# Kernel optimization log

Hardware: AMD Instinct MI355X
Metric: run time of the kernel (lower is better)

## Reference

```python
import jax, jax.numpy as jnp
import numpy as np

HIGHEST = jax.lax.Precision.HIGHEST
KEY_CHUNK_SIZE = 4096 * 4  # hard-coded in the module's __call__
HEADS = 8
DIM_HEAD = 64


def _query_chunk_size(num_q: int) -> int:
    # replicates the module's static chunk-size selection
    if num_q % 64 == 0:
        return num_q // 64
    if num_q % 16 == 0:
        return num_q // 16
    if num_q % 4 == 0:
        return num_q // 4
    return num_q


def _me_attention(q, k, v, q_chunk: int, k_chunk: int):
    # q, k, v: (S, H, D) where H here is the flattened batch*heads axis
    S, H, D = q.shape
    num_kv = k.shape[0]
    k_chunk = min(k_chunk, num_kv)
    q = q / jnp.sqrt(jnp.asarray(D, q.dtype))
    kc = k.reshape(-1, k_chunk, H, D)          # (nk, kc, H, D)
    vc = v.reshape(-1, k_chunk, H, v.shape[-1])

    def per_qchunk(qch):  # qch: (qc, H, D)
        def summarize(args):
            kch, vch = args
            s = jnp.einsum('qhd,khd->qhk', qch, kch, precision=HIGHEST)
            m = jax.lax.stop_gradient(jnp.max(s, axis=-1, keepdims=True))
            e = jnp.exp(s - m)
            ev = jnp.einsum('khf,qhk->qhf', vch, e, precision=HIGHEST)
            return ev, e.sum(axis=-1), m[..., 0]
        evs, ews, ms = jax.lax.map(summarize, (kc, vc))  # stacked over key chunks
        gm = jnp.max(ms, axis=0)                # (qc, H) global running max
        sc = jnp.exp(ms - gm)                   # (nk, qc, H) rescale factors
        num = (evs * sc[..., None]).sum(axis=0)
        den = (ews * sc).sum(axis=0)
        return num / den[..., None]

    qs = q.reshape(-1, q_chunk, H, D)
    out = jax.lax.map(per_qchunk, qs)           # (nq, qc, H, F)
    return out.reshape(S, H, -1)


def _forward(hidden_states, w_q, w_k, w_v, w_out, b_out):
    B, S, Dm = hidden_states.shape
    H, dh = HEADS, DIM_HEAD
    q = hidden_states @ w_q
    k = hidden_states @ w_k
    v = hidden_states @ w_v

    def to_heads(t):  # (B,S,H*dh) -> (B*H, S, dh)
        return t.reshape(B, S, H, dh).transpose(0, 2, 1, 3).reshape(B * H, S, dh)

    qs, ks, vs = to_heads(q), to_heads(k), to_heads(v)
    # module transposes to (S, B*H, dh) before memory-efficient attention
    qcs = _query_chunk_size(S)
    attn = _me_attention(qs.transpose(1, 0, 2), ks.transpose(1, 0, 2),
                         vs.transpose(1, 0, 2), qcs, KEY_CHUNK_SIZE)
    attn = attn.transpose(1, 0, 2)  # (B*H, S, dh)
    attn = attn.reshape(B, H, S, dh).transpose(0, 2, 1, 3).reshape(B, S, H * dh)
    return attn @ w_out + b_out


def setup_inputs() -> dict:
    key = jax.random.key(0)
    ks = jax.random.split(key, 6)
    B, S, Dm = 2, 8192, 512
    inner = HEADS * DIM_HEAD  # 512
    return {
        'hidden_states': jax.random.normal(ks[0], (B, S, Dm), dtype=jnp.float32),
        'w_q': jax.random.normal(ks[1], (Dm, inner), dtype=jnp.float32) * 0.02,
        'w_k': jax.random.normal(ks[2], (Dm, inner), dtype=jnp.float32) * 0.02,
        'w_v': jax.random.normal(ks[3], (Dm, inner), dtype=jnp.float32) * 0.02,
        'w_out': jax.random.normal(ks[4], (inner, Dm), dtype=jnp.float32) * 0.02,
        'b_out': jnp.zeros((Dm,), dtype=jnp.float32),
    }


def reference(hidden_states, w_q, w_k, w_v, w_out, b_out):
    return _forward(hidden_states, w_q, w_k, w_v, w_out, b_out)
```

## Files before the change

kernel.cpp:

```cpp
#include <hip/hip_runtime.h>
#include <stdint.h>

typedef unsigned short u16;
typedef __attribute__((ext_vector_type(8))) short short8;
typedef __attribute__((ext_vector_type(4))) short short4v;
typedef __attribute__((ext_vector_type(4))) float f32x4;

#define MFMA16(a, b, c) __builtin_amdgcn_mfma_f32_16x16x16bf16_1k(a, b, c, 0, 0, 0)
#define MFMA32(a, b, c) __builtin_amdgcn_mfma_f32_16x16x32_bf16(a, b, c, 0, 0, 0)

#if __has_builtin(__builtin_amdgcn_exp2f)
#define EXP2F(x) __builtin_amdgcn_exp2f(x)
#else
#define EXP2F(x) exp2f(x)
#endif

#define ASYNC16(G, L)                                                            \
    __builtin_amdgcn_global_load_lds((const __attribute__((address_space(1))) void*)(const void*)(G), \
                                     (__attribute__((address_space(3))) void*)(void*)(L), 16, 0, 0)

__device__ __forceinline__ u16 f2bf(float f) {
    union { float f; uint32_t u; } c; c.f = f;
    uint32_t r = (c.u + 0x7fffu + ((c.u >> 16) & 1u)) >> 16;
    return (u16)r;
}

__global__ __launch_bounds__(256) void k_convert_x(const float* __restrict__ X, u16* __restrict__ Xb) {
    int idx = blockIdx.x * 256 + threadIdx.x;
    float4 v = ((const float4*)X)[idx];
    union { u16 s[4]; uint2 v; } u;
    u.s[0] = f2bf(v.x); u.s[1] = f2bf(v.y); u.s[2] = f2bf(v.z); u.s[3] = f2bf(v.w);
    ((uint2*)Xb)[idx] = u.v;
}

__global__ __launch_bounds__(256) void k_convert_w(const float* __restrict__ W0, const float* __restrict__ W1,
                                                   const float* __restrict__ W2, const float* __restrict__ W3,
                                                   u16* __restrict__ Wt) {
    __shared__ u16 T[64][72];
    const float* W = (blockIdx.z == 0) ? W0 : (blockIdx.z == 1) ? W1 : (blockIdx.z == 2) ? W2 : W3;
    int k0 = blockIdx.x * 64, n0 = blockIdx.y * 64;
    int t = threadIdx.x;
    for (int i = 0; i < 4; i++) {
        int id = t + i * 256;
        int row = id >> 4, c4 = (id & 15) * 4;
        float4 v = *(const float4*)(W + (size_t)(k0 + row) * 512 + n0 + c4);
        union { u16 s[4]; uint2 v; } u;
        u.s[0] = f2bf(v.x); u.s[1] = f2bf(v.y); u.s[2] = f2bf(v.z); u.s[3] = f2bf(v.w);
        *(uint2*)&T[row][c4] = u.v;
    }
    __syncthreads();
    u16* O = Wt + (size_t)blockIdx.z * 512 * 512;
    for (int i = 0; i < 2; i++) {
        int id = t + i * 256;
        int row = id >> 3, c8 = (id & 7) * 8;
        union { u16 s[8]; uint4 v; } tmp;
        for (int j = 0; j < 8; j++) tmp.s[j] = T[c8 + j][row];
        *(uint4*)(O + (size_t)(n0 + row) * 512 + k0 + c8) = tmp.v;
    }
}

__global__ __launch_bounds__(256) void k_gemm_qkv(const u16* __restrict__ X, const u16* __restrict__ Wt,
                                                  u16* __restrict__ Q, u16* __restrict__ K, u16* __restrict__ V) {
    __shared__ u16 As[128][40];
    __shared__ u16 Bs[128][40];
    const int t = threadIdx.x;
    const int wave = t >> 6, lane = t & 63, quad = lane >> 4, l16 = lane & 15;
    const int wm = (wave >> 1) * 64, wn = (wave & 1) * 64;
    const int m0 = blockIdx.x * 128, n0 = blockIdx.y * 128;
    const u16* Bt = Wt + (size_t)blockIdx.z * 262144;
    const f32x4 fz = {0.f, 0.f, 0.f, 0.f};
    f32x4 acc[4][4];
    for (int i = 0; i < 4; i++) for (int j = 0; j < 4; j++) acc[i][j] = fz;
    for (int k0 = 0; k0 < 512; k0 += 32) {
        __syncthreads();
        for (int i = 0; i < 2; i++) {
            int id = t + i * 256;
            int row = id >> 2, c8 = (id & 3) * 8;
            *(uint4*)&As[row][c8] = *(const uint4*)(X + (size_t)(m0 + row) * 512 + k0 + c8);
            *(uint4*)&Bs[row][c8] = *(const uint4*)(Bt + (size_t)(n0 + row) * 512 + k0 + c8);
        }
        __syncthreads();
        short8 af[4], bf[4];
        for (int mt = 0; mt < 4; mt++) af[mt] = *(const short8*)&As[wm + mt * 16 + l16][quad * 8];
        for (int nt = 0; nt < 4; nt++) bf[nt] = *(const short8*)&Bs[wn + nt * 16 + l16][quad * 8];
        for (int mt = 0; mt < 4; mt++)
            for (int nt = 0; nt < 4; nt++)
                acc[mt][nt] = MFMA32(af[mt], bf[nt], acc[mt][nt]);
    }
    const float scale = (blockIdx.z == 0) ? 0.18033688011112042f : 1.0f;
    u16* Out = (blockIdx.z == 0) ? Q : (blockIdx.z == 1) ? K : V;
    for (int mt = 0; mt < 4; mt++)
        for (int nt = 0; nt < 4; nt++)
            for (int r = 0; r < 4; r++) {
                int m = m0 + wm + mt * 16 + quad * 4 + r;
                int n = n0 + wn + nt * 16 + l16;
                int b = m >> 13, s = m & 8191, h = n >> 6, d = n & 63;
                Out[((size_t)((b * 8 + h) * 8192 + s)) * 64 + d] = f2bf(acc[mt][nt][r] * scale);
            }
}

__global__ __launch_bounds__(256) void k_transpose_v(const u16* __restrict__ V, u16* __restrict__ Vt) {
    __shared__ u16 T[64][72];
    int s0 = blockIdx.x * 64, bh = blockIdx.y;
    int t = threadIdx.x;
    for (int i = 0; i < 2; i++) {
        int id = t + i * 256, row = id >> 3, c8 = (id & 7) * 8;
        *(uint4*)&T[row][c8] = *(const uint4*)(V + ((size_t)bh * 8192 + s0 + row) * 64 + c8);
    }
    __syncthreads();
    for (int i = 0; i < 2; i++) {
        int id = t + i * 256, row = id >> 3, c8 = (id & 7) * 8;
        union { u16 s[8]; uint4 v; } tmp;
        for (int j = 0; j < 8; j++) tmp.s[j] = T[c8 + j][row];
        *(uint4*)(Vt + ((size_t)bh * 64 + row) * 8192 + s0 + c8) = tmp.v;
    }
}

__global__ __launch_bounds__(512, 4) void k_flash(const u16* __restrict__ Q, const u16* __restrict__ K,
                                                  const u16* __restrict__ Vt, u16* __restrict__ Attn) {
    __shared__ u16 KsAll[2][4096];
    __shared__ u16 VsAll[2][4096];
    const int t = threadIdx.x;
    const int wave = t >> 6, lane = t & 63, quad = lane >> 4, l16 = lane & 15;
    const int l7 = l16 & 7, q1 = quad >> 1, qlo = quad & 1;
    const int qblk = blockIdx.x, bh = blockIdx.y;
    const int b = bh >> 3, h = bh & 7;
    const int q0g = qblk * 256;
    const int mq = wave * 32;
    const u16* Qb = Q + ((size_t)bh * 8192 + q0g) * 64;
    const u16* Kb = K + (size_t)bh * 8192 * 64;
    const u16* Vb = Vt + (size_t)bh * 64 * 8192;

    const int r0 = t >> 3;
    const int x0 = ((t & 7) ^ (r0 & 7)) * 8;
    const u16* gK0 = Kb + r0 * 64 + x0;
    const u16* gV0 = Vb + (size_t)r0 * 8192 + x0;
    u16* lK = &KsAll[0][0] + t * 8;
    u16* lV = &VsAll[0][0] + t * 8;

    auto prefetch = [&](int it, int buf) {
        ASYNC16(gK0 + it * 4096, lK + buf * 4096);
        ASYNC16(gV0 + it * 64,   lV + buf * 4096);
    };

    short8 qf[2][2];
    for (int mt = 0; mt < 2; mt++)
        for (int ks = 0; ks < 2; ks++)
            qf[mt][ks] = *(const short8*)(Qb + (size_t)(mq + mt * 16 + l16) * 64 + ks * 32 + quad * 8);

    const f32x4 fz = {0.f, 0.f, 0.f, 0.f};
    f32x4 o[2][4];
    float l_i[2] = {0.f, 0.f};
    for (int mt = 0; mt < 2; mt++) for (int nt = 0; nt < 4; nt++) o[mt][nt] = fz;

    prefetch(0, 0);

    auto body = [&](int it, int buf) {
        __syncthreads();
        if (it != 127) prefetch(it + 1, buf ^ 1);
        const u16* KsB = &KsAll[buf][0];
        const u16* VsB = &VsAll[buf][0];

        f32x4 sc[2][4];
        for (int kt = 0; kt < 4; kt++) {
            short8 kf0 = *(const short8*)(KsB + kt * 1024 + l16 * 64 + (((0 * 4 + quad) ^ l7) * 8));
            short8 kf1 = *(const short8*)(KsB + kt * 1024 + l16 * 64 + (((1 * 4 + quad) ^ l7) * 8));
            sc[0][kt] = MFMA32(kf0, qf[0][0], fz);
            sc[1][kt] = MFMA32(kf0, qf[1][0], fz);
            sc[0][kt] = MFMA32(kf1, qf[0][1], sc[0][kt]);
            sc[1][kt] = MFMA32(kf1, qf[1][1], sc[1][kt]);
        }

        short4v pf[2][4];
        for (int mt = 0; mt < 2; mt++)
            for (int kt = 0; kt < 4; kt++) {
                union { float f; uint32_t u; } e0, e1, e2, e3;
                e0.f = EXP2F(sc[mt][kt][0]);
                e1.f = EXP2F(sc[mt][kt][1]);
                e2.f = EXP2F(sc[mt][kt][2]);
                e3.f = EXP2F(sc[mt][kt][3]);
                l_i[mt] += (e0.f + e1.f) + (e2.f + e3.f);
                union { uint32_t u[2]; short4v s; } pk;
                pk.u[0] = __builtin_amdgcn_perm(e1.u, e0.u, 0x07060302);
                pk.u[1] = __builtin_amdgcn_perm(e3.u, e2.u, 0x07060302);
                pf[mt][kt] = pk.s;
            }

        for (int kt = 0; kt < 4; kt++)
            for (int nt = 0; nt < 4; nt++) {
                short4v vf = *(const short4v*)(VsB + nt * 1024 + l16 * 64 + (((kt * 2 + q1) ^ l7) * 8) + qlo * 4);
                o[0][nt] = MFMA16(pf[0][kt], vf, o[0][nt]);
                o[1][nt] = MFMA16(pf[1][kt], vf, o[1][nt]);
            }
    };

    for (int it2 = 0; it2 < 64; it2++) {
        body(2 * it2, 0);
        body(2 * it2 + 1, 1);
    }

    for (int mt = 0; mt < 2; mt++) {
        float l = l_i[mt];
        l += __shfl_xor(l, 16);
        l += __shfl_xor(l, 32);
        float inv = 1.0f / l;
        float invC[4];
        for (int r = 0; r < 4; r++) invC[r] = __shfl(inv, quad * 4 + r);
        for (int nt = 0; nt < 4; nt++)
            for (int r = 0; r < 4; r++) {
                int sg = q0g + mq + mt * 16 + quad * 4 + r;
                int n = h * 64 + nt * 16 + l16;
                Attn[((size_t)(b * 8192 + sg)) * 512 + n] = f2bf(o[mt][nt][r] * invC[r]);
            }
    }
}

__global__ __launch_bounds__(256) void k_gemm_out(const u16* __restrict__ A, const u16* __restrict__ Wot,
                                                  const float* __restrict__ bias, float* __restrict__ Out) {
    __shared__ u16 As[128][40];
    __shared__ u16 Bs[128][40];
    const int t = threadIdx.x;
    const int wave = t >> 6, lane = t & 63, quad = lane >> 4, l16 = lane & 15;
    const int wm = (wave >> 1) * 64, wn = (wave & 1) * 64;
    const int m0 = blockIdx.x * 128, n0 = blockIdx.y * 128;
    const f32x4 fz = {0.f, 0.f, 0.f, 0.f};
    f32x4 acc[4][4];
    for (int i = 0; i < 4; i++) for (int j = 0; j < 4; j++) acc[i][j] = fz;
    for (int k0 = 0; k0 < 512; k0 += 32) {
        __syncthreads();
        for (int i = 0; i < 2; i++) {
            int id = t + i * 256;
            int row = id >> 2, c8 = (id & 3) * 8;
            *(uint4*)&As[row][c8] = *(const uint4*)(A + (size_t)(m0 + row) * 512 + k0 + c8);
            *(uint4*)&Bs[row][c8] = *(const uint4*)(Wot + (size_t)(n0 + row) * 512 + k0 + c8);
        }
        __syncthreads();
        short8 af[4], bf[4];
        for (int mt = 0; mt < 4; mt++) af[mt] = *(const short8*)&As[wm + mt * 16 + l16][quad * 8];
        for (int nt = 0; nt < 4; nt++) bf[nt] = *(const short8*)&Bs[wn + nt * 16 + l16][quad * 8];
        for (int mt = 0; mt < 4; mt++)
            for (int nt = 0; nt < 4; nt++)
                acc[mt][nt] = MFMA32(af[mt], bf[nt], acc[mt][nt]);
    }
    float bv[4];
    for (int nt = 0; nt < 4; nt++) bv[nt] = bias[n0 + wn + nt * 16 + l16];
    for (int mt = 0; mt < 4; mt++)
        for (int nt = 0; nt < 4; nt++)
            for (int r = 0; r < 4; r++) {
                int m = m0 + wm + mt * 16 + quad * 4 + r;
                int n = n0 + wn + nt * 16 + l16;
                Out[(size_t)m * 512 + n] = acc[mt][nt][r] + bv[nt];
            }
}

extern "C" void kernel_launch(void* const* d_in, const int* in_sizes, int n_in,
                              void* d_out, int out_size, void* d_ws, size_t ws_size,
                              hipStream_t stream) {
    const float* X   = (const float*)d_in[0];
    const float* w_q = (const float*)d_in[1];
    const float* w_k = (const float*)d_in[2];
    const float* w_v = (const float*)d_in[3];
    const float* w_o = (const float*)d_in[4];
    const float* b_o = (const float*)d_in[5];
    float* Out = (float*)d_out;

    char* ws = (char*)d_ws;
    u16* Xb   = (u16*)(ws);
    u16* Wt   = (u16*)(ws + 16777216);
    u16* Qd   = (u16*)(ws + 18874368);
    u16* Kd   = (u16*)(ws + 35651584);
    u16* Vd   = (u16*)(ws + 52428800);
    u16* Vtd  = (u16*)(ws + 69206016);
    u16* Attn = Xb;

    hipLaunchKernelGGL(k_convert_x, dim3(8192), dim3(256), 0, stream, X, Xb);
    hipLaunchKernelGGL(k_convert_w, dim3(8, 8, 4), dim3(256), 0, stream, w_q, w_k, w_v, w_o, Wt);
    hipLaunchKernelGGL(k_gemm_qkv, dim3(128, 4, 3), dim3(256), 0, stream, Xb, Wt, Qd, Kd, Vd);
    hipLaunchKernelGGL(k_transpose_v, dim3(128, 16), dim3(256), 0, stream, Vd, Vtd);
    hipLaunchKernelGGL(k_flash, dim3(32, 16), dim3(512), 0, stream, Qd, Kd, Vtd, Attn);
    hipLaunchKernelGGL(k_gemm_out, dim3(128, 4), dim3(256), 0, stream, Attn, Wt + 3 * 262144, b_o, Out);
}
```

Baseline: 433.3 us.

## Give each flash-attention wave 64 query rows with 4 waves per block

The flash kernel now runs 256 threads (4 waves) per block, and each wave handles 64 query rows instead of 32. Each K/V fragment read from LDS therefore feeds twice as many MFMAs. Score computation and exp/pack are interleaved per key tile, and the grid is reordered so that blocks for the same query tile run back-to-back across heads. The cost is higher register pressure (the launch bound drops to 2 blocks per CU) and fewer waves sharing each LDS tile, which means more prefetch loads per thread.

```diff
diff --git a/kernel.cpp b/kernel.cpp
--- a/kernel.cpp
+++ b/kernel.cpp
@@ -116,42 +116,47 @@
     }
 }
 
-__global__ __launch_bounds__(512, 4) void k_flash(const u16* __restrict__ Q, const u16* __restrict__ K,
+__global__ __launch_bounds__(256, 2) void k_flash(const u16* __restrict__ Q, const u16* __restrict__ K,
                                                   const u16* __restrict__ Vt, u16* __restrict__ Attn) {
     __shared__ u16 KsAll[2][4096];
     __shared__ u16 VsAll[2][4096];
     const int t = threadIdx.x;
     const int wave = t >> 6, lane = t & 63, quad = lane >> 4, l16 = lane & 15;
     const int l7 = l16 & 7, q1 = quad >> 1, qlo = quad & 1;
-    const int qblk = blockIdx.x, bh = blockIdx.y;
+    const int bh = blockIdx.x, qblk = blockIdx.y;
     const int b = bh >> 3, h = bh & 7;
     const int q0g = qblk * 256;
-    const int mq = wave * 32;
+    const int mq = wave * 64;
     const u16* Qb = Q + ((size_t)bh * 8192 + q0g) * 64;
     const u16* Kb = K + (size_t)bh * 8192 * 64;
     const u16* Vb = Vt + (size_t)bh * 64 * 8192;
 
-    const int r0 = t >> 3;
+    const int r0 = t >> 3, r1 = (t + 256) >> 3;
     const int x0 = ((t & 7) ^ (r0 & 7)) * 8;
+    const int x1 = ((t & 7) ^ (r1 & 7)) * 8;
     const u16* gK0 = Kb + r0 * 64 + x0;
+    const u16* gK1 = Kb + r1 * 64 + x1;
     const u16* gV0 = Vb + (size_t)r0 * 8192 + x0;
+    const u16* gV1 = Vb + (size_t)r1 * 8192 + x1;
     u16* lK = &KsAll[0][0] + t * 8;
     u16* lV = &VsAll[0][0] + t * 8;
 
     auto prefetch = [&](int it, int buf) {
         ASYNC16(gK0 + it * 4096, lK + buf * 4096);
+        ASYNC16(gK1 + it * 4096, lK + buf * 4096 + 2048);
         ASYNC16(gV0 + it * 64,   lV + buf * 4096);
+        ASYNC16(gV1 + it * 64,   lV + buf * 4096 + 2048);
     };
 
-    short8 qf[2][2];
-    for (int mt = 0; mt < 2; mt++)
+    short8 qf[4][2];
+    for (int mt = 0; mt < 4; mt++)
         for (int ks = 0; ks < 2; ks++)
             qf[mt][ks] = *(const short8*)(Qb + (size_t)(mq + mt * 16 + l16) * 64 + ks * 32 + quad * 8);
 
     const f32x4 fz = {0.f, 0.f, 0.f, 0.f};
-    f32x4 o[2][4];
-    float l_i[2] = {0.f, 0.f};
-    for (int mt = 0; mt < 2; mt++) for (int nt = 0; nt < 4; nt++) o[mt][nt] = fz;
+    f32x4 o[4][4];
+    float l_i[4] = {0.f, 0.f, 0.f, 0.f};
+    for (int mt = 0; mt < 4; mt++) for (int nt = 0; nt < 4; nt++) o[mt][nt] = fz;
 
     prefetch(0, 0);
 
@@ -161,36 +166,33 @@
         const u16* KsB = &KsAll[buf][0];
         const u16* VsB = &VsAll[buf][0];
 
-        f32x4 sc[2][4];
+        short4v pf[4][4];
         for (int kt = 0; kt < 4; kt++) {
             short8 kf0 = *(const short8*)(KsB + kt * 1024 + l16 * 64 + (((0 * 4 + quad) ^ l7) * 8));
             short8 kf1 = *(const short8*)(KsB + kt * 1024 + l16 * 64 + (((1 * 4 + quad) ^ l7) * 8));
-            sc[0][kt] = MFMA32(kf0, qf[0][0], fz);
-            sc[1][kt] = MFMA32(kf0, qf[1][0], fz);
-            sc[0][kt] = MFMA32(kf1, qf[0][1], sc[0][kt]);
-            sc[1][kt] = MFMA32(kf1, qf[1][1], sc[1][kt]);
-        }
-
-        short4v pf[2][4];
-        for (int mt = 0; mt < 2; mt++)
-            for (int kt = 0; kt < 4; kt++) {
+            for (int mt = 0; mt < 4; mt++) {
+                f32x4 sc = MFMA32(kf0, qf[mt][0], fz);
+                sc = MFMA32(kf1, qf[mt][1], sc);
                 union { float f; uint32_t u; } e0, e1, e2, e3;
-                e0.f = EXP2F(sc[mt][kt][0]);
-                e1.f = EXP2F(sc[mt][kt][1]);
-                e2.f = EXP2F(sc[mt][kt][2]);
-                e3.f = EXP2F(sc[mt][kt][3]);
+                e0.f = EXP2F(sc[0]);
+                e1.f = EXP2F(sc[1]);
+                e2.f = EXP2F(sc[2]);
+                e3.f = EXP2F(sc[3]);
                 l_i[mt] += (e0.f + e1.f) + (e2.f + e3.f);
                 union { uint32_t u[2]; short4v s; } pk;
                 pk.u[0] = __builtin_amdgcn_perm(e1.u, e0.u, 0x07060302);
                 pk.u[1] = __builtin_amdgcn_perm(e3.u, e2.u, 0x07060302);
                 pf[mt][kt] = pk.s;
             }
+        }
 
         for (int kt = 0; kt < 4; kt++)
             for (int nt = 0; nt < 4; nt++) {
                 short4v vf = *(const short4v*)(VsB + nt * 1024 + l16 * 64 + (((kt * 2 + q1) ^ l7) * 8) + qlo * 4);
                 o[0][nt] = MFMA16(pf[0][kt], vf, o[0][nt]);
                 o[1][nt] = MFMA16(pf[1][kt], vf, o[1][nt]);
+                o[2][nt] = MFMA16(pf[2][kt], vf, o[2][nt]);
+                o[3][nt] = MFMA16(pf[3][kt], vf, o[3][nt]);
             }
     };
 
@@ -199,7 +201,7 @@
         body(2 * it2 + 1, 1);
     }
 
-    for (int mt = 0; mt < 2; mt++) {
+    for (int mt = 0; mt < 4; mt++) {
         float l = l_i[mt];
         l += __shfl_xor(l, 16);
         l += __shfl_xor(l, 32);
@@ -277,6 +279,6 @@
     hipLaunchKernelGGL(k_convert_w, dim3(8, 8, 4), dim3(256), 0, stream, w_q, w_k, w_v, w_o, Wt);
     hipLaunchKernelGGL(k_gemm_qkv, dim3(128, 4, 3), dim3(256), 0, stream, Xb, Wt, Qd, Kd, Vd);
     hipLaunchKernelGGL(k_transpose_v, dim3(128, 16), dim3(256), 0, stream, Vd, Vtd);
-    hipLaunchKernelGGL(k_flash, dim3(32, 16), dim3(512), 0, stream, Qd, Kd, Vtd, Attn);
+    hipLaunchKernelGGL(k_flash, dim3(16, 32), dim3(256), 0, stream, Qd, Kd, Vtd, Attn);
     hipLaunchKernelGGL(k_gemm_out, dim3(128, 4), dim3(256), 0, stream, Attn, Wt + 3 * 262144, b_o, Out);
 }
```

Result: no change. 440.8 us (+1.7%).
